# Optimization experiments

Hardware: AMD Instinct MI355X
Metric: run time of the kernel (lower is better)

## Reference

```python
import jax, jax.numpy as jnp
import numpy as np

VOCAB = 10000
X_DIM = 128
HID = 256


def setup_inputs() -> dict:
    key = jax.random.key(0)
    ks = jax.random.split(key, 8)
    B, S = 128, 50
    x = jax.random.randint(ks[0], (B, S), 0, VOCAB, dtype=jnp.int32).astype(jnp.int64)
    emb = jax.random.normal(ks[1], (VOCAB, X_DIM), dtype=jnp.float32) * 0.02
    # PyTorch nn.RNN params: W_ih [H, X], W_hh [H, H], b_ih [H], b_hh [H]
    W_ih = jax.random.normal(ks[2], (HID, X_DIM), dtype=jnp.float32) * (1.0 / np.sqrt(HID))
    W_hh = jax.random.normal(ks[3], (HID, HID), dtype=jnp.float32) * (1.0 / np.sqrt(HID))
    b_ih = jax.random.normal(ks[4], (HID,), dtype=jnp.float32) * 0.01
    b_hh = jax.random.normal(ks[5], (HID,), dtype=jnp.float32) * 0.01
    # nn.Linear: W_aff [V, H], b_aff [V]
    W_aff = jax.random.normal(ks[6], (VOCAB, HID), dtype=jnp.float32) * (1.0 / np.sqrt(HID))
    b_aff = jax.random.normal(ks[7], (VOCAB,), dtype=jnp.float32) * 0.01
    return {"x": x, "emb": emb, "W_ih": W_ih, "W_hh": W_hh,
            "b_ih": b_ih, "b_hh": b_hh, "W_aff": W_aff, "b_aff": b_aff}


def reference(x, emb, W_ih, W_hh, b_ih, b_hh, W_aff, b_aff):
    B, S = x.shape
    embs = emb[x]                                    # [B, S, X]
    # Precompute input projection for all timesteps (batched GEMM)
    xin = jnp.einsum('bsx,hx->bsh', embs, W_ih) + b_ih + b_hh  # [B, S, H]
    h0 = jnp.zeros((B, HID), dtype=embs.dtype)

    def step(h, xt):
        h = jnp.tanh(xt + h @ W_hh.T)
        return h, h

    _, hs = jax.lax.scan(step, h0, jnp.swapaxes(xin, 0, 1))  # hs: [S, B, H]
    hs = jnp.swapaxes(hs, 0, 1)                              # [B, S, H]
    ys = jnp.einsum('bsh,vh->bsv', hs, W_aff) + b_aff        # [B, S, V]
    return ys
```

## Files before the change

### kernel.cpp

```cpp
#include <hip/hip_runtime.h>
#include <hip/hip_bf16.h>
#include <stdint.h>

#define VOCAB 10000
#define XDIM 128
#define HID 256
#define BATCH 128
#define SEQ 50
#define ROWS (BATCH * SEQ)

#define BM 128
#define BN 256
#define BK 64
#define NTM 50
#define NTN 40

#define K1_BLOCKS (ROWS / 8)
#define K0_BLOCKS ((VOCAB * HID) / (256 * 8))

typedef __bf16 bf16x8 __attribute__((ext_vector_type(8)));
typedef float f32x4 __attribute__((ext_vector_type(4)));

__device__ __forceinline__ uint16_t f2bf(float f) {
    union { float f; uint32_t i; } v;
    v.f = f;
    uint32_t x = v.i;
    return (uint16_t)((x + 0x7fffu + ((x >> 16) & 1u)) >> 16);
}

__global__ __launch_bounds__(256, 2) void k01_fused(
    const int* __restrict__ x, const float* __restrict__ emb,
    const float* __restrict__ Wih, const float* __restrict__ bih,
    const float* __restrict__ bhh, float* __restrict__ xin,
    const float* __restrict__ Waff, uint16_t* __restrict__ Wb) {
    __shared__ __align__(16) float es[8][XDIM];
    const int tid = threadIdx.x;

    if (blockIdx.x >= K1_BLOCKS) {
        const int i = ((blockIdx.x - K1_BLOCKS) * 256 + tid) * 8;
        float4 a = *(const float4*)(Waff + i);
        float4 b = *(const float4*)(Waff + i + 4);
        uint16_t t[8];
        t[0] = f2bf(a.x); t[1] = f2bf(a.y); t[2] = f2bf(a.z); t[3] = f2bf(a.w);
        t[4] = f2bf(b.x); t[5] = f2bf(b.y); t[6] = f2bf(b.z); t[7] = f2bf(b.w);
        *(uint4*)(Wb + i) = *(const uint4*)t;
        return;
    }

    const int r0 = blockIdx.x * 8;
    {
        const int row = tid >> 5, c = tid & 31;
        const int tok = x[r0 + row];
        *(float4*)&es[row][c * 4] = *(const float4*)(emb + tok * XDIM + c * 4);
    }
    __syncthreads();

    const int j = tid;
    float wf[XDIM];
    const float4* wrow = (const float4*)(Wih + j * XDIM);
#pragma unroll
    for (int c = 0; c < 32; ++c) *(float4*)&wf[c * 4] = wrow[c];
    const float bias = bih[j] + bhh[j];

    float acc[8];
#pragma unroll
    for (int r = 0; r < 8; ++r) acc[r] = bias;
#pragma unroll
    for (int k4 = 0; k4 < 32; ++k4) {
#pragma unroll
        for (int r = 0; r < 8; ++r) {
            float4 e = *(const float4*)&es[r][k4 * 4];
            acc[r] += e.x * wf[k4 * 4 + 0] + e.y * wf[k4 * 4 + 1] +
                      e.z * wf[k4 * 4 + 2] + e.w * wf[k4 * 4 + 3];
        }
    }
#pragma unroll
    for (int r = 0; r < 8; ++r) xin[(r0 + r) * HID + j] = acc[r];
}

__global__ __launch_bounds__(512, 2) void k2_rnn(
    const float* __restrict__ xin, const float* __restrict__ Whh,
    uint16_t* __restrict__ hs) {
    __shared__ __align__(16) float hb[HID];
    __shared__ float ps[HID];
    const int b = blockIdx.x;
    const int j = threadIdx.x & 255;
    const int half = threadIdx.x >> 8;

    float wh[128];
    const float4* wrow = (const float4*)(Whh + j * HID + half * 128);
#pragma unroll
    for (int c = 0; c < 32; ++c) *(float4*)&wh[c * 4] = wrow[c];

    if (threadIdx.x < HID) hb[threadIdx.x] = 0.0f;
    __syncthreads();

    const float* xr = xin + b * SEQ * HID;
    uint16_t* hr = hs + b * SEQ * HID;

    for (int t = 0; t < SEQ; ++t) {
        const float xv = xr[t * HID + j];
        const float4* h4 = (const float4*)(hb + half * 128);
        float a0 = 0.f, a1 = 0.f, a2 = 0.f, a3 = 0.f;
#pragma unroll
        for (int c = 0; c < 32; ++c) {
            float4 v = h4[c];
            a0 += v.x * wh[c * 4 + 0];
            a1 += v.y * wh[c * 4 + 1];
            a2 += v.z * wh[c * 4 + 2];
            a3 += v.w * wh[c * 4 + 3];
        }
        const float part = (a0 + a1) + (a2 + a3);
        if (half) ps[j] = part;
        __syncthreads();
        if (!half) {
            const float hn = tanhf(part + ps[j] + xv);
            hb[j] = hn;
            hr[t * HID + j] = f2bf(hn);
        }
        __syncthreads();
    }
}

__global__ __launch_bounds__(256, 2) void k3_gemm(
    const uint16_t* __restrict__ A,
    const uint16_t* __restrict__ Bw,
    const float* __restrict__ baff,
    float* __restrict__ out) {
    __shared__ __align__(16) char smem[49152];
    uint16_t* As = (uint16_t*)smem;
    uint16_t* Bs = (uint16_t*)(smem + BM * BK * 2);

    const int bid0 = blockIdx.x;
    const int bid = (bid0 & 7) * ((NTM * NTN) / 8) + (bid0 >> 3);
    const int bm = bid % NTM, bn = bid / NTM;
    const int m0 = bm * BM, n0 = bn * BN;
    const int tid = threadIdx.x;
    const int wv = tid >> 6, ln = tid & 63;
    const int wm = wv & 1, wn = wv >> 1;
    const int quad = ln >> 4, l15 = ln & 15;

    f32x4 acc[4][8];
#pragma unroll
    for (int i = 0; i < 4; ++i)
#pragma unroll
        for (int jj = 0; jj < 8; ++jj) acc[i][jj] = (f32x4)0.0f;

    const int lrow = ln >> 3;
    const int gsw = ((ln & 7) ^ lrow) * 8;

    for (int kt = 0; kt < 4; ++kt) {
        const int k0 = kt * BK;
#pragma unroll
        for (int i = 0; i < 4; ++i) {
            const int ci = wv * 4 + i;
            const uint16_t* g = A + (size_t)(m0 + ci * 8 + lrow) * HID + k0 + gsw;
            __builtin_amdgcn_global_load_lds(
                (const __attribute__((address_space(1))) void*)g,
                (__attribute__((address_space(3))) void*)(As + ci * 512), 16, 0, 0);
        }
#pragma unroll
        for (int i = 0; i < 8; ++i) {
            const int ci = wv * 8 + i;
            int n = n0 + ci * 8 + lrow;
            if (n > VOCAB - 1) n = VOCAB - 1;
            const uint16_t* g = Bw + (size_t)n * HID + k0 + gsw;
            __builtin_amdgcn_global_load_lds(
                (const __attribute__((address_space(1))) void*)g,
                (__attribute__((address_space(3))) void*)(Bs + ci * 512), 16, 0, 0);
        }
        __syncthreads();

#pragma unroll
        for (int kk = 0; kk < 2; ++kk) {
            const int gk = kk * 4 + quad;
            bf16x8 af[4], bf[8];
#pragma unroll
            for (int tm = 0; tm < 4; ++tm) {
                const int R = wm * 64 + tm * 16 + l15;
                af[tm] = *(const bf16x8*)&As[R * 64 + ((gk ^ (R & 7)) * 8)];
            }
#pragma unroll
            for (int tn = 0; tn < 8; ++tn) {
                const int R = wn * 128 + tn * 16 + l15;
                bf[tn] = *(const bf16x8*)&Bs[R * 64 + ((gk ^ (R & 7)) * 8)];
            }
#pragma unroll
            for (int tm = 0; tm < 4; ++tm)
#pragma unroll
                for (int tn = 0; tn < 8; ++tn)
                    acc[tm][tn] = __builtin_amdgcn_mfma_f32_16x16x32_bf16(
                        af[tm], bf[tn], acc[tm][tn], 0, 0, 0);
        }
        __syncthreads();
    }

    float* csw = (float*)smem + wv * 16 * 132;
    float bias[8];
#pragma unroll
    for (int tn = 0; tn < 8; ++tn) {
        int n = n0 + wn * 128 + tn * 16 + l15;
        bias[tn] = baff[n > VOCAB - 1 ? VOCAB - 1 : n];
    }
#pragma unroll
    for (int tm = 0; tm < 4; ++tm) {
#pragma unroll
        for (int tn = 0; tn < 8; ++tn)
#pragma unroll
            for (int r = 0; r < 4; ++r)
                csw[(quad * 4 + r) * 132 + tn * 16 + l15] =
                    acc[tm][tn][r] + bias[tn];
        __syncthreads();
#pragma unroll
        for (int it = 0; it < 8; ++it) {
            const int row = it * 2 + (ln >> 5);
            const int c4 = (ln & 31) * 4;
            const f32x4 v = *(const f32x4*)&csw[row * 132 + c4];
            const int gm = m0 + wm * 64 + tm * 16 + row;
            const int gn = n0 + wn * 128 + c4;
            if (gn < VOCAB)
                __builtin_nontemporal_store(
                    v, (f32x4*)(out + (size_t)gm * VOCAB + gn));
        }
        __syncthreads();
    }
}

extern "C" void kernel_launch(void* const* d_in, const int* in_sizes, int n_in,
                              void* d_out, int out_size, void* d_ws, size_t ws_size,
                              hipStream_t stream) {
    const int* x = (const int*)d_in[0];
    const float* emb = (const float*)d_in[1];
    const float* Wih = (const float*)d_in[2];
    const float* Whh = (const float*)d_in[3];
    const float* bih = (const float*)d_in[4];
    const float* bhh = (const float*)d_in[5];
    const float* Waff = (const float*)d_in[6];
    const float* baff = (const float*)d_in[7];

    float* xin = (float*)d_ws;
    uint16_t* hsb = (uint16_t*)((char*)d_ws + (size_t)ROWS * HID * 4);
    uint16_t* Wb = hsb + (size_t)ROWS * HID;
    float* out = (float*)d_out;

    k01_fused<<<K1_BLOCKS + K0_BLOCKS, 256, 0, stream>>>(
        x, emb, Wih, bih, bhh, xin, Waff, Wb);
    k2_rnn<<<BATCH, 512, 0, stream>>>(xin, Whh, hsb);
    k3_gemm<<<NTM * NTN, 256, 0, stream>>>(hsb, Wb, baff, out);
}
```

Baseline: 360.3 us.

## Run RNN recurrence on MFMA with split-bf16 precision, 16 batches per block

The recurrent step now runs as bf16 MFMA matrix multiplies over 16 batch rows per block instead of one batch per block with fp32 scalar dot products. To keep close to fp32 accuracy, W_hh and h are each split into high and low bf16 parts and three MFMAs are issued per product. The hidden state is double-buffered in LDS, so each step needs one barrier instead of two. The cost is that only 8 blocks run on the GPU, which leaves most CUs idle, and the split-precision products give slightly different numerics.

```diff
diff --git a/kernel.cpp b/kernel.cpp
--- a/kernel.cpp
+++ b/kernel.cpp
@@ -18,6 +18,10 @@
 #define K1_BLOCKS (ROWS / 8)
 #define K0_BLOCKS ((VOCAB * HID) / (256 * 8))
 
+#define K2G 16
+#define K2_BLOCKS (BATCH / K2G)
+#define HPAD 264
+
 typedef __bf16 bf16x8 __attribute__((ext_vector_type(8)));
 typedef float f32x4 __attribute__((ext_vector_type(4)));
 
@@ -26,6 +30,11 @@
     v.f = f;
     uint32_t x = v.i;
     return (uint16_t)((x + 0x7fffu + ((x >> 16) & 1u)) >> 16);
+}
+__device__ __forceinline__ float bf2f(uint16_t b) {
+    union { uint32_t u; float f; } v;
+    v.u = (uint32_t)b << 16;
+    return v.f;
 }
 
 __global__ __launch_bounds__(256, 2) void k01_fused(
@@ -81,42 +90,94 @@
 __global__ __launch_bounds__(512, 2) void k2_rnn(
     const float* __restrict__ xin, const float* __restrict__ Whh,
     uint16_t* __restrict__ hs) {
-    __shared__ __align__(16) float hb[HID];
-    __shared__ float ps[HID];
-    const int b = blockIdx.x;
-    const int j = threadIdx.x & 255;
-    const int half = threadIdx.x >> 8;
-
-    float wh[128];
-    const float4* wrow = (const float4*)(Whh + j * HID + half * 128);
-#pragma unroll
-    for (int c = 0; c < 32; ++c) *(float4*)&wh[c * 4] = wrow[c];
-
-    if (threadIdx.x < HID) hb[threadIdx.x] = 0.0f;
+    __shared__ __align__(16) uint16_t H[2][2][K2G][HPAD];
+
+    const int tid = threadIdx.x;
+    const int wave = tid >> 6, ln = tid & 63;
+    const int quad = ln >> 4, l15 = ln & 15;
+    const int g0 = blockIdx.x * K2G;
+
+    bf16x8 whi[2][8], wlo[2][8];
+#pragma unroll
+    for (int nt = 0; nt < 2; ++nt) {
+        const int j = wave * 32 + nt * 16 + l15;
+#pragma unroll
+        for (int ks = 0; ks < 8; ++ks) {
+            float w[8];
+            const float* wp = Whh + (size_t)j * HID + ks * 32 + quad * 8;
+            *(float4*)&w[0] = *(const float4*)(wp);
+            *(float4*)&w[4] = *(const float4*)(wp + 4);
+            uint16_t hb_[8], lb_[8];
+#pragma unroll
+            for (int v = 0; v < 8; ++v) {
+                hb_[v] = f2bf(w[v]);
+                lb_[v] = f2bf(w[v] - bf2f(hb_[v]));
+            }
+            whi[nt][ks] = *(const bf16x8*)hb_;
+            wlo[nt][ks] = *(const bf16x8*)lb_;
+        }
+    }
+
+#pragma unroll
+    for (int nt = 0; nt < 2; ++nt) {
+        const int j = wave * 32 + nt * 16 + l15;
+#pragma unroll
+        for (int r = 0; r < 4; ++r) {
+            const int lb = quad * 4 + r;
+            const size_t row = (size_t)(g0 + lb) * SEQ + 0;
+            const float hv = tanhf(xin[row * HID + j]);
+            const uint16_t hi = f2bf(hv);
+            H[0][0][lb][j] = hi;
+            H[0][1][lb][j] = f2bf(hv - bf2f(hi));
+            hs[row * HID + j] = hi;
+        }
+    }
     __syncthreads();
 
-    const float* xr = xin + b * SEQ * HID;
-    uint16_t* hr = hs + b * SEQ * HID;
-
-    for (int t = 0; t < SEQ; ++t) {
-        const float xv = xr[t * HID + j];
-        const float4* h4 = (const float4*)(hb + half * 128);
-        float a0 = 0.f, a1 = 0.f, a2 = 0.f, a3 = 0.f;
-#pragma unroll
-        for (int c = 0; c < 32; ++c) {
-            float4 v = h4[c];
-            a0 += v.x * wh[c * 4 + 0];
-            a1 += v.y * wh[c * 4 + 1];
-            a2 += v.z * wh[c * 4 + 2];
-            a3 += v.w * wh[c * 4 + 3];
-        }
-        const float part = (a0 + a1) + (a2 + a3);
-        if (half) ps[j] = part;
-        __syncthreads();
-        if (!half) {
-            const float hn = tanhf(part + ps[j] + xv);
-            hb[j] = hn;
-            hr[t * HID + j] = f2bf(hn);
+    for (int t = 1; t < SEQ; ++t) {
+        const int cur = (t - 1) & 1, nxt = t & 1;
+
+        float xv[2][4];
+#pragma unroll
+        for (int nt = 0; nt < 2; ++nt) {
+            const int j = wave * 32 + nt * 16 + l15;
+#pragma unroll
+            for (int r = 0; r < 4; ++r) {
+                const size_t row = (size_t)(g0 + quad * 4 + r) * SEQ + t;
+                xv[nt][r] = xin[row * HID + j];
+            }
+        }
+
+        f32x4 c[2] = {(f32x4)0.0f, (f32x4)0.0f};
+#pragma unroll
+        for (int ks = 0; ks < 8; ++ks) {
+            const bf16x8 ah =
+                *(const bf16x8*)&H[cur][0][l15][ks * 32 + quad * 8];
+            const bf16x8 al =
+                *(const bf16x8*)&H[cur][1][l15][ks * 32 + quad * 8];
+#pragma unroll
+            for (int nt = 0; nt < 2; ++nt) {
+                c[nt] = __builtin_amdgcn_mfma_f32_16x16x32_bf16(
+                    ah, whi[nt][ks], c[nt], 0, 0, 0);
+                c[nt] = __builtin_amdgcn_mfma_f32_16x16x32_bf16(
+                    al, whi[nt][ks], c[nt], 0, 0, 0);
+                c[nt] = __builtin_amdgcn_mfma_f32_16x16x32_bf16(
+                    ah, wlo[nt][ks], c[nt], 0, 0, 0);
+            }
+        }
+
+#pragma unroll
+        for (int nt = 0; nt < 2; ++nt) {
+            const int j = wave * 32 + nt * 16 + l15;
+#pragma unroll
+            for (int r = 0; r < 4; ++r) {
+                const int lb = quad * 4 + r;
+                const float hv = tanhf(c[nt][r] + xv[nt][r]);
+                const uint16_t hi = f2bf(hv);
+                H[nxt][0][lb][j] = hi;
+                H[nxt][1][lb][j] = f2bf(hv - bf2f(hi));
+                hs[((size_t)(g0 + lb) * SEQ + t) * HID + j] = hi;
+            }
         }
         __syncthreads();
     }
@@ -245,6 +306,6 @@
 
     k01_fused<<<K1_BLOCKS + K0_BLOCKS, 256, 0, stream>>>(
         x, emb, Wih, bih, bhh, xin, Waff, Wb);
-    k2_rnn<<<BATCH, 512, 0, stream>>>(xin, Whh, hsb);
+    k2_rnn<<<K2_BLOCKS, 512, 0, stream>>>(xin, Whh, hsb);
     k3_gemm<<<NTM * NTN, 256, 0, stream>>>(hsb, Wb, baff, out);
 }
```

New measurement: 417.2 us. +15.8%, slower.
